# Optimization experiments

Measured on AMD Instinct MI355X. Metric: run time of the kernel, lower is better.

The kernel has to match this reference:

```python
import math
import jax, jax.numpy as jnp
import numpy as np

D, H, NB, L, K = 45, 256, 6, 2, 8          # features, hidden, maf blocks, made hidden layers, spline bins
M = 3 * K - 1                               # params per feature (tails='linear')
TAIL = -math.log(1e-6)                      # tail_bound = -log(alpha)
MIN_BW = MIN_BH = MIN_D = 1e-3


def _masks():
    # nflows MADE sequential degrees (random_mask=False)
    d_in = np.arange(1, D + 1)
    d_h = (np.arange(H) % (D - 1)) + 1
    m0 = (d_h[:, None] >= d_in[None, :]).astype(np.float32)   # [H, D]
    mh = (d_h[:, None] >= d_h[None, :]).astype(np.float32)    # [H, H]
    d_out = np.repeat(d_in, M)                                 # nflows tile(): each degree repeated M times
    mf = (d_out[:, None] > d_h[None, :]).astype(np.float32)   # [D*M, H], strict for output layer
    return jnp.asarray(m0), jnp.asarray(mh), jnp.asarray(mf)


def _rq_spline(x, params):
    # x: [B, D]; params: [B, D, M]. unconstrained_rational_quadratic_spline, tails='linear'.
    uw = params[..., :K] / math.sqrt(H)        # nflows divides by sqrt(hidden_features)
    uh = params[..., K:2 * K] / math.sqrt(H)
    const = math.log(math.exp(1.0 - MIN_D) - 1.0)
    ud = jnp.pad(params[..., 2 * K:], ((0, 0), (0, 0), (1, 1)), constant_values=const)  # [B,D,K+1]
    inside = (x >= -TAIL) & (x <= TAIL)
    xc = jnp.clip(x, -TAIL, TAIL)

    def bin_edges(u, mn):
        p = jax.nn.softmax(u, -1)
        p = mn + (1.0 - mn * K) * p
        c = jnp.pad(jnp.cumsum(p, -1), ((0, 0), (0, 0), (1, 0)))
        c = 2.0 * TAIL * c - TAIL
        c = c.at[..., 0].set(-TAIL).at[..., -1].set(TAIL)
        return c, c[..., 1:] - c[..., :-1]

    cw, w = bin_edges(uw, MIN_BW)              # cumwidths [B,D,K+1], widths [B,D,K]
    ch, h = bin_edges(uh, MIN_BH)
    d = MIN_D + jax.nn.softplus(ud)            # derivatives [B,D,K+1]

    idx = jnp.clip(jnp.sum((xc[..., None] >= cw), -1) - 1, 0, K - 1)[..., None]
    g = lambda a: jnp.take_along_axis(a, idx, -1)[..., 0]
    icw, ibw, ich, ih = g(cw[..., :-1]), g(w), g(ch[..., :-1]), g(h)
    idelta = g(h / w)
    id0, id1 = g(d[..., :-1]), g(d[..., 1:])

    th = (xc - icw) / ibw
    th1 = th * (1.0 - th)
    den = idelta + (id0 + id1 - 2.0 * idelta) * th1
    y = ich + ih * (idelta * th * th + id0 * th1) / den
    lad = jnp.log(idelta * idelta * (id1 * th * th + 2.0 * idelta * th1 + id0 * (1.0 - th) ** 2)) - 2.0 * jnp.log(den)
    return jnp.where(inside, y, x), jnp.where(inside, lad, 0.0)


def setup_inputs() -> dict:
    key = jax.random.key(0)
    ks = jax.random.split(key, 10)
    B, s = 32768, 0.02
    return {
        "x": jax.random.normal(ks[0], (B, D), jnp.float32),
        "cond": jax.random.normal(ks[1], (B, 1), jnp.float32),
        "W0": jax.random.normal(ks[2], (NB, H, D), jnp.float32) * s,
        "b0": jax.random.normal(ks[3], (NB, H), jnp.float32) * s,
        "Wc": jax.random.normal(ks[4], (NB, H, 1), jnp.float32) * s,
        "bc": jax.random.normal(ks[5], (NB, H), jnp.float32) * s,
        "Wh": jax.random.normal(ks[6], (NB, L, H, H), jnp.float32) * s,
        "bh": jax.random.normal(ks[7], (NB, L, H), jnp.float32) * s,
        "Wf": jax.random.normal(ks[8], (NB, D * M, H), jnp.float32) * s,
        "bf": jax.random.normal(ks[9], (NB, D * M), jnp.float32) * s,
    }


def reference(x, cond, W0, b0, Wc, bc, Wh, bh, Wf, bf):
    m0, mh, mf = _masks()
    z = x
    ld = jnp.zeros(x.shape[0], x.dtype)
    for b in range(NB):  # CompositeTransform of NB MAF blocks
        hid = z @ (W0[b] * m0).T + b0[b] + cond @ Wc[b].T + bc[b]
        for l in range(L):  # MaskedFeedforwardBlock: linear -> ReLU (dropout=0, no BN)
            hid = jax.nn.relu(hid @ (Wh[b, l] * mh).T + bh[b, l])
        params = (hid @ (Wf[b] * mf).T + bf[b]).reshape(z.shape[0], D, M)
        z, lad = _rq_spline(z, params)
        ld = ld + lad.sum(-1)
    log_z = 0.5 * D * math.log(2.0 * math.pi)
    return -0.5 * jnp.sum(z * z, axis=1) - log_z + ld
```

## Files before the change

### kernel.cpp

```cpp
#include <hip/hip_runtime.h>


typedef __bf16 bf16;
typedef __bf16 bf16x8 __attribute__((ext_vector_type(8)));
typedef float  f32x16 __attribute__((ext_vector_type(16)));

#define TAILF  13.815510557964274f
#define LOGZ   41.352233994210265f

#define WS_W0M   0
#define WS_WHM   196608
#define WS_WFM   1769472
#define WS_BEFF  5210112
#define WS_BFP   5216256
#define WS_WCC   5243136
#define WS_BHP   5249280
#define WS_NEED  5261568

#define N_W0  (6*256*64)
#define N_WH  (6*2*256*256)
#define N_WF  (6*5*224*256)
#define N_PREP (N_W0 + N_WH + N_WF)

__device__ __forceinline__ int s_deg(int s) {
    return (s < 216) ? (s / 6) : (36 + (s - 216) / 5);
}
__device__ __forceinline__ int s_orig(int s) {
    int d, rk;
    if (s < 216) { d = s / 6; rk = s - d * 6; }
    else { int u = s - 216; d = 36 + u / 5; rk = u - (u / 5) * 5; }
    return d + 44 * rk;
}

__global__ void prep_all(const float* __restrict__ W0, const float* __restrict__ b0,
                         const float* __restrict__ Wc, const float* __restrict__ bc,
                         const float* __restrict__ Wh, const float* __restrict__ Wf,
                         const float* __restrict__ bfv, const float* __restrict__ bh,
                         bf16* __restrict__ W0m, bf16* __restrict__ Whm,
                         bf16* __restrict__ Wfm,
                         float* __restrict__ beff, float* __restrict__ bfp,
                         float* __restrict__ Wcc, float* __restrict__ bhp)
{
    int idx = blockIdx.x * 256 + threadIdx.x;
    if (idx < N_W0) {
        int j = idx & 7, lane = (idx >> 3) & 63, chunk = idx >> 9;
        int kt = chunk & 3, cg = (chunk >> 2) & 7, b = chunk >> 5;
        int col = cg * 32 + (lane & 31);
        int k   = kt * 16 + (lane >> 5) * 8 + j;
        int o   = s_orig(col);
        float v = 0.f;
        if (k < 45 && s_deg(col) >= k)
            v = W0[(b * 256 + o) * 45 + k];
        W0m[idx] = (bf16)v;
        if (k == 0) {
            beff[b * 256 + col] = b0[b * 256 + o] + bc[b * 256 + o];
            Wcc[b * 256 + col]  = Wc[b * 256 + o];
        }
    } else if (idx < N_W0 + N_WH) {
        int id = idx - N_W0;
        int j = id & 7, lane = (id >> 3) & 63, chunk = id >> 9;
        int kt = chunk & 15, cg = (chunk >> 4) & 7, bl = chunk >> 7;
        int col = cg * 32 + (lane & 31);
        int k   = kt * 16 + (lane >> 5) * 8 + j;
        int oc  = s_orig(col), ok = s_orig(k);
        float v = (s_deg(col) >= s_deg(k)) ? Wh[bl * 65536 + oc * 256 + ok] : 0.f;
        Whm[id] = (bf16)v;
        if (k == 0)
            bhp[bl * 256 + col] = bh[bl * 256 + oc];
    } else if (idx < N_PREP) {
        int id = idx - (N_W0 + N_WH);
        int j = id & 7, lane = (id >> 3) & 63, chunk = id >> 9;
        int kt = chunk & 15, t2 = chunk >> 4;
        int cg = t2 % 7, bg = t2 / 7;
        int b  = bg / 5, g = bg - 5 * b;
        int col = cg * 32 + (lane & 31);
        int k   = kt * 16 + (lane >> 5) * 8 + j;
        int ok  = s_orig(k);
        int f   = 9 * g + col / 23;
        int m   = col - (col / 23) * 23;
        bool valid = (col < 207);
        float v = 0.f;
        if (valid && (f > s_deg(k)))
            v = Wf[(b * 1035 + f * 23 + m) * 256 + ok];
        Wfm[id] = (bf16)v;
        if (k == 0)
            bfp[bg * 224 + col] = valid ? bfv[b * 1035 + f * 23 + m] : 0.f;
    }
}

#define SO_ZF    0
#define SO_ZB    11776
#define SO_HIDA  18944
#define SO_PBUF  52736
#define SO_COND  80528
#define SO_LD    80784
#define SMEM_BYTES 81040

#define PBF 1544

#define E2(c0,h0,k0,c1,h1,k1) \
    ( (unsigned)(((k0)<<8)|((h0)<<5)|(c0)) | ((unsigned)(((k1)<<8)|((h1)<<5)|(c1))<<16) )

__constant__ unsigned SCHED_IN[8] = {
    E2(6,0,3, 0,0,1), E2(6,1,3, 0,1,1), E2(7,0,3, 1,0,1), E2(7,1,3, 1,1,1),
    E2(3,0,2, 2,0,1), E2(3,1,2, 2,1,1), E2(4,0,2, 5,0,2), E2(4,1,2, 5,1,2)
};
__constant__ unsigned SCHED_HID[8] = {
    E2(7,0,16, 0,0,3), E2(7,1,16, 0,1,3), E2(6,0,15, 1,0,5), E2(6,1,15, 1,1,5),
    E2(5,0,12, 2,0,6), E2(5,1,12, 2,1,6), E2(4,0,11, 3,0,9), E2(4,1,11, 3,1,9)
};
__constant__ unsigned SCHED_OUT[5][8] = {
  { E2(4,0,3, 0,0,1),  E2(4,1,3, 0,1,1),  E2(5,0,3, 1,0,1),  E2(5,1,3, 1,1,1),
    E2(6,0,3, 31,0,0), E2(6,1,3, 31,0,0), E2(2,0,2, 2,1,2),  E2(3,0,2, 3,1,2) },
  { E2(5,0,7, 0,0,4),  E2(5,1,7, 0,1,4),  E2(6,0,7, 31,0,0), E2(6,1,7, 31,0,0),
    E2(3,0,6, 1,0,5),  E2(3,1,6, 1,1,5),  E2(4,0,6, 2,0,5),  E2(4,1,6, 2,1,5) },
  { E2(5,0,10, 0,0,8), E2(5,1,10, 0,1,8), E2(6,0,10, 1,0,8), E2(6,1,10, 1,1,8),
    E2(2,0,9, 2,1,9),  E2(3,0,9, 3,1,9),  E2(4,0,9, 31,0,0), E2(4,1,9, 31,0,0) },
  { E2(5,0,14, 0,0,11),E2(5,1,14, 0,1,11),E2(6,0,14, 31,0,0),E2(6,1,14, 31,0,0),
    E2(4,0,13, 1,0,11),E2(4,1,13, 1,1,11),E2(2,0,12, 2,1,12),E2(3,0,12, 3,1,12) },
  { E2(3,0,16, 0,0,14),E2(3,1,16, 0,1,14),E2(4,0,16, 1,0,15),E2(4,1,16, 1,1,15),
    E2(5,0,16, 2,0,15),E2(5,1,16, 2,1,15),E2(6,0,16, 31,0,0),E2(6,1,16, 31,0,0) }
};

template<int MODE>
__device__ __forceinline__ void epi32(const f32x16& acc, int cg, int hf,
    const float* __restrict__ bias, const float* __restrict__ wcol,
    const float* condl, bf16* dst, int l31, int kh8)
{
    const int col = cg * 32 + l31;
    if (MODE == 2 && col >= 207) return;
    const float bv = bias[col];
    const int rb = (kh8 >> 1) + hf * 32;
    if (MODE == 2) {
        const int fl = col / 23, m = col - fl * 23;
        bf16* dp = dst + fl * PBF + m;
        #pragma unroll
        for (int r = 0; r < 16; ++r) {
            int row = (r & 3) + 8 * (r >> 2) + rb;
            dp[row * 24] = (bf16)(acc[r] + bv);
        }
    } else {
        const float wcv = (MODE == 0) ? wcol[col] : 0.f;
        #pragma unroll
        for (int r = 0; r < 16; ++r) {
            int row = (r & 3) + 8 * (r >> 2) + rb;
            float v = acc[r] + bv;
            if (MODE == 0) v += condl[row] * wcv;
            if (MODE == 1) v = fmaxf(v, 0.f);
            dst[row * 264 + col] = (bf16)v;
        }
    }
}

template<int KTFULL, int MODE>
__device__ __forceinline__ void gemm32(
    const bf16* Asrc, const int lda,
    const bf16* __restrict__ Wp,
    const float* __restrict__ bias, const float* __restrict__ wcol,
    const float* condl, bf16* dst,
    const unsigned* __restrict__ sched,
    int w, int lane, bool preEpiSync)
{
    const int l31 = lane & 31;
    const int kh8 = (lane >> 5) * 8;
    const unsigned se = sched[__builtin_amdgcn_readfirstlane(w)];
    const int cg0 = se & 31,         hf0 = (se >> 5) & 1,  kt0 = (se >> 8) & 31;
    const int cg1 = (se >> 16) & 31, hf1 = (se >> 21) & 1, kt1 = (se >> 24) & 31;

    f32x16 acc0 = {}, acc1 = {};
    {
        const bf16* Bp = Wp + (size_t)cg0 * (KTFULL * 512) + lane * 8;
        const bf16* Ap = Asrc + (hf0 * 32 + l31) * lda + kh8;
        #pragma unroll 1
        for (int kb = 0; kb < kt0; kb += 4) {
            bf16x8 bq[4], aq[4];
            #pragma unroll
            for (int c = 0; c < 4; ++c) if (kb + c < kt0) {
                bq[c] = *reinterpret_cast<const bf16x8*>(Bp + (kb + c) * 512);
                aq[c] = *reinterpret_cast<const bf16x8*>(Ap + (kb + c) * 16);
            }
            #pragma unroll
            for (int c = 0; c < 4; ++c) if (kb + c < kt0)
                acc0 = __builtin_amdgcn_mfma_f32_32x32x16_bf16(aq[c], bq[c], acc0, 0, 0, 0);
        }
    }
    {
        const bf16* Bp = Wp + (size_t)cg1 * (KTFULL * 512) + lane * 8;
        const bf16* Ap = Asrc + (hf1 * 32 + l31) * lda + kh8;
        #pragma unroll 1
        for (int kb = 0; kb < kt1; kb += 4) {
            bf16x8 bq[4], aq[4];
            #pragma unroll
            for (int c = 0; c < 4; ++c) if (kb + c < kt1) {
                bq[c] = *reinterpret_cast<const bf16x8*>(Bp + (kb + c) * 512);
                aq[c] = *reinterpret_cast<const bf16x8*>(Ap + (kb + c) * 16);
            }
            #pragma unroll
            for (int c = 0; c < 4; ++c) if (kb + c < kt1)
                acc1 = __builtin_amdgcn_mfma_f32_32x32x16_bf16(aq[c], bq[c], acc1, 0, 0, 0);
        }
    }

    if (preEpiSync) __syncthreads();

    if (cg0 != 31) epi32<MODE>(acc0, cg0, hf0, bias, wcol, condl, dst, l31, kh8);
    if (cg1 != 31) epi32<MODE>(acc1, cg1, hf1, bias, wcol, condl, dst, l31, kh8);
    __syncthreads();
}

__device__ __forceinline__ void do_spline9(int fb, float* zf, bf16* zb,
                                           const bf16* pbuf, int t, float& lad_acc)
{
    #pragma unroll 1
    for (int task = t; task < 576; task += 512) {
        int fl = task >> 6, r = task & 63;
        const bf16* pp = pbuf + fl * PBF + r * 24;
        bf16x8 q0 = *reinterpret_cast<const bf16x8*>(pp);
        bf16x8 q1 = *reinterpret_cast<const bf16x8*>(pp + 8);
        bf16x8 q2 = *reinterpret_cast<const bf16x8*>(pp + 16);
        float P[23];
        #pragma unroll
        for (int m = 0; m < 8; ++m) P[m]      = (float)q0[m];
        #pragma unroll
        for (int m = 0; m < 8; ++m) P[8 + m]  = (float)q1[m];
        #pragma unroll
        for (int m = 0; m < 7; ++m) P[16 + m] = (float)q2[m];

        float xin = zf[r * 46 + fb + fl];
        float xc  = fminf(fmaxf(xin, -TAILF), TAILF);
        bool inside = (xin >= -TAILF) && (xin <= TAILF);

        float mw = P[0];
        #pragma unroll
        for (int i = 1; i < 8; ++i) mw = fmaxf(mw, P[i]);
        float ew[8], sw = 0.f;
        #pragma unroll
        for (int i = 0; i < 8; ++i) { ew[i] = __expf((P[i] - mw) * 0.0625f); sw += ew[i]; }
        float rws = 0.992f / sw;
        float cw[9]; cw[0] = -TAILF;
        #pragma unroll
        for (int i = 0; i < 8; ++i)
            cw[i + 1] = cw[i] + 2.f * TAILF * (1e-3f + ew[i] * rws);
        cw[8] = TAILF;
        float wb[8];
        #pragma unroll
        for (int i = 0; i < 8; ++i) wb[i] = cw[i + 1] - cw[i];

        float mh = P[8];
        #pragma unroll
        for (int i = 1; i < 8; ++i) mh = fmaxf(mh, P[8 + i]);
        float eh[8], sh = 0.f;
        #pragma unroll
        for (int i = 0; i < 8; ++i) { eh[i] = __expf((P[8 + i] - mh) * 0.0625f); sh += eh[i]; }
        float rhs = 0.992f / sh;
        float ch[9]; ch[0] = -TAILF;
        #pragma unroll
        for (int i = 0; i < 8; ++i)
            ch[i + 1] = ch[i] + 2.f * TAILF * (1e-3f + eh[i] * rhs);
        ch[8] = TAILF;
        float hb[8];
        #pragma unroll
        for (int i = 0; i < 8; ++i) hb[i] = ch[i + 1] - ch[i];

        float dd[9];
        dd[0] = 1.0f; dd[8] = 1.0f;
        #pragma unroll
        for (int i = 1; i < 8; ++i)
            dd[i] = 1e-3f + __logf(1.f + __expf(P[15 + i]));

        float icw = cw[0], ich = ch[0], ibw = wb[0], ibh = hb[0];
        float id0 = dd[0], id1 = dd[1];
        #pragma unroll
        for (int i = 1; i < 8; ++i) {
            bool ge = xc >= cw[i];
            icw = ge ? cw[i] : icw;  ich = ge ? ch[i] : ich;
            ibw = ge ? wb[i] : ibw;  ibh = ge ? hb[i] : ibh;
            id0 = ge ? dd[i] : id0;  id1 = ge ? dd[i + 1] : id1;
        }

        float th  = (xc - icw) / ibw;
        float th1 = th * (1.f - th);
        float dl  = ibh / ibw;
        float den = dl + (id0 + id1 - 2.f * dl) * th1;
        float yy  = ich + ibh * (dl * th * th + id0 * th1) / den;
        float num = dl * dl * (id1 * th * th + 2.f * dl * th1
                               + id0 * (1.f - th) * (1.f - th));
        float lad = __logf(num) - 2.f * __logf(den);

        if (inside) {
            zf[r * 46 + fb + fl] = yy;
            zb[r * 56 + fb + fl] = (bf16)yy;
        }
        lad_acc += inside ? lad : 0.f;
    }
}

__global__ __launch_bounds__(512, 4) void maf_main(
    const float* __restrict__ x, const float* __restrict__ cond,
    const bf16* __restrict__ W0m, const bf16* __restrict__ Whm,
    const bf16* __restrict__ Wfm,
    const float* __restrict__ beff, const float* __restrict__ bfp,
    const float* __restrict__ Wcc, const float* __restrict__ bhp,
    float* __restrict__ out, int B)
{
    extern __shared__ char smem[];
    float* zf    = (float*)(smem + SO_ZF);
    bf16*  zb    = (bf16*)(smem + SO_ZB);
    bf16*  hidA  = (bf16*)(smem + SO_HIDA);
    bf16*  pbuf  = (bf16*)(smem + SO_PBUF);
    float* condl = (float*)(smem + SO_COND);
    float* ldl   = (float*)(smem + SO_LD);

    const int t    = threadIdx.x;
    const int r0   = blockIdx.x * 64;
    const int w    = t >> 6;
    const int lane = t & 63;

    for (int i = t; i < 64 * 11; i += 512) {
        int r = i / 11, c = i - (i / 11) * 11;
        zb[r * 56 + 45 + c] = (bf16)0.f;
    }
    for (int i = t; i < 64 * 45; i += 512) {
        int r = i / 45, f = i - (i / 45) * 45;
        float v = (r0 + r < B) ? x[(size_t)(r0 + r) * 45 + f] : 0.f;
        zf[r * 46 + f] = v;
        zb[r * 56 + f] = (bf16)v;
    }
    if (t < 64) {
        condl[t] = (r0 + t < B) ? cond[r0 + t] : 0.f;
        ldl[t]   = 0.f;
    }
    __syncthreads();

    float lad_acc = 0.f;

    #pragma unroll 1
    for (int b = 0; b < 6; ++b) {
        gemm32<4, 0>(zb, 56, W0m + b * 16384,
                     beff + b * 256, Wcc + b * 256, condl,
                     hidA, SCHED_IN, w, lane, false);
        #pragma unroll 1
        for (int l = 0; l < 2; ++l)
            gemm32<16, 1>(hidA, 264, Whm + (b * 2 + l) * 65536,
                          bhp + (b * 2 + l) * 256, nullptr, condl,
                          hidA, SCHED_HID, w, lane, true);
        #pragma unroll 1
        for (int g = 0; g < 5; ++g) {
            gemm32<16, 2>(hidA, 264, Wfm + (size_t)(b * 5 + g) * 57344,
                          bfp + (b * 5 + g) * 224, nullptr, condl,
                          pbuf, SCHED_OUT[g], w, lane, false);
            do_spline9(g * 9, zf, zb, pbuf, t, lad_acc);
            __syncthreads();
        }
    }

    atomicAdd(&ldl[t & 63], lad_acc);
    __syncthreads();

    if (t < 64 && r0 + t < B) {
        float s = 0.f;
        #pragma unroll
        for (int f = 0; f < 45; ++f) { float v = zf[t * 46 + f]; s += v * v; }
        out[r0 + t] = -0.5f * s - LOGZ + ldl[t];
    }
}

extern "C" void kernel_launch(void* const* d_in, const int* in_sizes, int n_in,
                              void* d_out, int out_size, void* d_ws, size_t ws_size,
                              hipStream_t stream)
{
    const float* x    = (const float*)d_in[0];
    const float* cond = (const float*)d_in[1];
    const float* W0   = (const float*)d_in[2];
    const float* b0   = (const float*)d_in[3];
    const float* Wc   = (const float*)d_in[4];
    const float* bc   = (const float*)d_in[5];
    const float* Wh   = (const float*)d_in[6];
    const float* bh   = (const float*)d_in[7];
    const float* Wf   = (const float*)d_in[8];
    const float* bfv  = (const float*)d_in[9];
    float* out = (float*)d_out;

    const int B = in_sizes[0] / 45;
    if (ws_size < (size_t)WS_NEED) return;

    char* ws = (char*)d_ws;
    bf16*  W0m  = (bf16*)(ws + WS_W0M);
    bf16*  Whm  = (bf16*)(ws + WS_WHM);
    bf16*  Wfm  = (bf16*)(ws + WS_WFM);
    float* beff = (float*)(ws + WS_BEFF);
    float* bfp  = (float*)(ws + WS_BFP);
    float* Wcc  = (float*)(ws + WS_WCC);
    float* bhp  = (float*)(ws + WS_BHP);

    prep_all<<<(N_PREP + 255) / 256, 256, 0, stream>>>(
        W0, b0, Wc, bc, Wh, Wf, bfv, bh, W0m, Whm, Wfm, beff, bfp, Wcc, bhp);

    (void)hipFuncSetAttribute((const void*)maf_main,
                              hipFuncAttributeMaxDynamicSharedMemorySize,
                              SMEM_BYTES);

    const int nwg = (B + 63) / 64;
    maf_main<<<nwg, 512, SMEM_BYTES, stream>>>(
        x, cond, W0m, Whm, Wfm, beff, bfp, Wcc, bhp, out, B);
}
```

Baseline: 366.9 us.

## Assign each wave a full 64-row column tile and software-pipeline B loads

Replaces the balanced per-wave schedule of two independent 32x32 tiles with one 32-column group per wave covering both 32-row halves, so each B fragment loaded from global memory feeds two MFMAs. The k-loop is replaced by a fully unrolled switch that double-buffers B register quads, issuing the next quad's loads before computing the current one. This halves weight traffic per MFMA and improves latency hiding, but drops the load-balanced schedule tables, so wave work is less even across the masked triangular K extents (waves 6/7 share a column group in the output GEMM).

```diff
diff --git a/kernel.cpp b/kernel.cpp
--- a/kernel.cpp
+++ b/kernel.cpp
@@ -98,29 +98,13 @@
 
 #define PBF 1544
 
-#define E2(c0,h0,k0,c1,h1,k1) \
-    ( (unsigned)(((k0)<<8)|((h0)<<5)|(c0)) | ((unsigned)(((k1)<<8)|((h1)<<5)|(c1))<<16) )
-
-__constant__ unsigned SCHED_IN[8] = {
-    E2(6,0,3, 0,0,1), E2(6,1,3, 0,1,1), E2(7,0,3, 1,0,1), E2(7,1,3, 1,1,1),
-    E2(3,0,2, 2,0,1), E2(3,1,2, 2,1,1), E2(4,0,2, 5,0,2), E2(4,1,2, 5,1,2)
-};
-__constant__ unsigned SCHED_HID[8] = {
-    E2(7,0,16, 0,0,3), E2(7,1,16, 0,1,3), E2(6,0,15, 1,0,5), E2(6,1,15, 1,1,5),
-    E2(5,0,12, 2,0,6), E2(5,1,12, 2,1,6), E2(4,0,11, 3,0,9), E2(4,1,11, 3,1,9)
-};
-__constant__ unsigned SCHED_OUT[5][8] = {
-  { E2(4,0,3, 0,0,1),  E2(4,1,3, 0,1,1),  E2(5,0,3, 1,0,1),  E2(5,1,3, 1,1,1),
-    E2(6,0,3, 31,0,0), E2(6,1,3, 31,0,0), E2(2,0,2, 2,1,2),  E2(3,0,2, 3,1,2) },
-  { E2(5,0,7, 0,0,4),  E2(5,1,7, 0,1,4),  E2(6,0,7, 31,0,0), E2(6,1,7, 31,0,0),
-    E2(3,0,6, 1,0,5),  E2(3,1,6, 1,1,5),  E2(4,0,6, 2,0,5),  E2(4,1,6, 2,1,5) },
-  { E2(5,0,10, 0,0,8), E2(5,1,10, 0,1,8), E2(6,0,10, 1,0,8), E2(6,1,10, 1,1,8),
-    E2(2,0,9, 2,1,9),  E2(3,0,9, 3,1,9),  E2(4,0,9, 31,0,0), E2(4,1,9, 31,0,0) },
-  { E2(5,0,14, 0,0,11),E2(5,1,14, 0,1,11),E2(6,0,14, 31,0,0),E2(6,1,14, 31,0,0),
-    E2(4,0,13, 1,0,11),E2(4,1,13, 1,1,11),E2(2,0,12, 2,1,12),E2(3,0,12, 3,1,12) },
-  { E2(3,0,16, 0,0,14),E2(3,1,16, 0,1,14),E2(4,0,16, 1,0,15),E2(4,1,16, 1,1,15),
-    E2(5,0,16, 2,0,15),E2(5,1,16, 2,1,15),E2(6,0,16, 31,0,0),E2(6,1,16, 31,0,0) }
-};
+__constant__ unsigned char HID_KT[8]    = {4,8,8,12,12,12,16,16};
+__constant__ unsigned char OUT_KT[5][7] = {
+    { 4, 4, 4, 4, 4, 4, 4},
+    { 4, 8, 8, 8, 8, 8, 8},
+    { 8, 8,12,12,12,12,12},
+    {12,12,12,12,16,16,16},
+    {16,16,16,16,16,16,16}};
 
 template<int MODE>
 __device__ __forceinline__ void epi32(const f32x16& acc, int cg, int hf,
@@ -153,58 +137,70 @@
 }
 
 template<int KTFULL, int MODE>
-__device__ __forceinline__ void gemm32(
+__device__ __forceinline__ void gemm64(
     const bf16* Asrc, const int lda,
     const bf16* __restrict__ Wp,
     const float* __restrict__ bias, const float* __restrict__ wcol,
     const float* condl, bf16* dst,
-    const unsigned* __restrict__ sched,
-    int w, int lane, bool preEpiSync)
+    int cg, int kt, int halfmask,
+    int lane, bool preEpiSync)
 {
     const int l31 = lane & 31;
     const int kh8 = (lane >> 5) * 8;
-    const unsigned se = sched[__builtin_amdgcn_readfirstlane(w)];
-    const int cg0 = se & 31,         hf0 = (se >> 5) & 1,  kt0 = (se >> 8) & 31;
-    const int cg1 = (se >> 16) & 31, hf1 = (se >> 21) & 1, kt1 = (se >> 24) & 31;
+    const bf16* Bp  = Wp + (size_t)cg * (KTFULL * 512) + lane * 8;
+    const bf16* Alo = Asrc + l31 * lda + kh8;
+    const bf16* Ahi = Alo + 32 * lda;
 
     f32x16 acc0 = {}, acc1 = {};
-    {
-        const bf16* Bp = Wp + (size_t)cg0 * (KTFULL * 512) + lane * 8;
-        const bf16* Ap = Asrc + (hf0 * 32 + l31) * lda + kh8;
-        #pragma unroll 1
-        for (int kb = 0; kb < kt0; kb += 4) {
-            bf16x8 bq[4], aq[4];
-            #pragma unroll
-            for (int c = 0; c < 4; ++c) if (kb + c < kt0) {
-                bq[c] = *reinterpret_cast<const bf16x8*>(Bp + (kb + c) * 512);
-                aq[c] = *reinterpret_cast<const bf16x8*>(Ap + (kb + c) * 16);
-            }
-            #pragma unroll
-            for (int c = 0; c < 4; ++c) if (kb + c < kt0)
-                acc0 = __builtin_amdgcn_mfma_f32_32x32x16_bf16(aq[c], bq[c], acc0, 0, 0, 0);
-        }
-    }
-    {
-        const bf16* Bp = Wp + (size_t)cg1 * (KTFULL * 512) + lane * 8;
-        const bf16* Ap = Asrc + (hf1 * 32 + l31) * lda + kh8;
-        #pragma unroll 1
-        for (int kb = 0; kb < kt1; kb += 4) {
-            bf16x8 bq[4], aq[4];
-            #pragma unroll
-            for (int c = 0; c < 4; ++c) if (kb + c < kt1) {
-                bq[c] = *reinterpret_cast<const bf16x8*>(Bp + (kb + c) * 512);
-                aq[c] = *reinterpret_cast<const bf16x8*>(Ap + (kb + c) * 16);
-            }
-            #pragma unroll
-            for (int c = 0; c < 4; ++c) if (kb + c < kt1)
-                acc1 = __builtin_amdgcn_mfma_f32_32x32x16_bf16(aq[c], bq[c], acc1, 0, 0, 0);
-        }
-    }
+    bf16x8 pA0, pA1, pA2, pA3, pB0, pB1, pB2, pB3;
+
+#define LB(c)  (*reinterpret_cast<const bf16x8*>(Bp + (c) * 512))
+#define LAL(c) (*reinterpret_cast<const bf16x8*>(Alo + (c) * 16))
+#define LAH(c) (*reinterpret_cast<const bf16x8*>(Ahi + (c) * 16))
+#define CHUNK(breg, c) { \
+    bf16x8 a0_ = LAL(c), a1_ = LAH(c); \
+    acc0 = __builtin_amdgcn_mfma_f32_32x32x16_bf16(a0_, breg, acc0, 0, 0, 0); \
+    acc1 = __builtin_amdgcn_mfma_f32_32x32x16_bf16(a1_, breg, acc1, 0, 0, 0); }
+#define LOADQ(r0, r1, r2, r3, q) { \
+    r0 = LB((q)*4 + 0); r1 = LB((q)*4 + 1); \
+    r2 = LB((q)*4 + 2); r3 = LB((q)*4 + 3); }
+#define COMPQ(r0, r1, r2, r3, q) { \
+    CHUNK(r0, (q)*4 + 0) CHUNK(r1, (q)*4 + 1) \
+    CHUNK(r2, (q)*4 + 2) CHUNK(r3, (q)*4 + 3) }
+
+    const int nq = __builtin_amdgcn_readfirstlane(kt >> 2);
+    switch (nq) {
+    case 1:
+        LOADQ(pA0,pA1,pA2,pA3, 0);
+        COMPQ(pA0,pA1,pA2,pA3, 0);
+        break;
+    case 2:
+        LOADQ(pA0,pA1,pA2,pA3, 0); LOADQ(pB0,pB1,pB2,pB3, 1);
+        COMPQ(pA0,pA1,pA2,pA3, 0); COMPQ(pB0,pB1,pB2,pB3, 1);
+        break;
+    case 3:
+        LOADQ(pA0,pA1,pA2,pA3, 0); LOADQ(pB0,pB1,pB2,pB3, 1);
+        COMPQ(pA0,pA1,pA2,pA3, 0); LOADQ(pA0,pA1,pA2,pA3, 2);
+        COMPQ(pB0,pB1,pB2,pB3, 1); COMPQ(pA0,pA1,pA2,pA3, 2);
+        break;
+    default:
+        LOADQ(pA0,pA1,pA2,pA3, 0); LOADQ(pB0,pB1,pB2,pB3, 1);
+        COMPQ(pA0,pA1,pA2,pA3, 0); LOADQ(pA0,pA1,pA2,pA3, 2);
+        COMPQ(pB0,pB1,pB2,pB3, 1); LOADQ(pB0,pB1,pB2,pB3, 3);
+        COMPQ(pA0,pA1,pA2,pA3, 2); COMPQ(pB0,pB1,pB2,pB3, 3);
+        break;
+    }
+#undef LB
+#undef LAL
+#undef LAH
+#undef CHUNK
+#undef LOADQ
+#undef COMPQ
 
     if (preEpiSync) __syncthreads();
 
-    if (cg0 != 31) epi32<MODE>(acc0, cg0, hf0, bias, wcol, condl, dst, l31, kh8);
-    if (cg1 != 31) epi32<MODE>(acc1, cg1, hf1, bias, wcol, condl, dst, l31, kh8);
+    if (halfmask & 1) epi32<MODE>(acc0, cg, 0, bias, wcol, condl, dst, l31, kh8);
+    if (halfmask & 2) epi32<MODE>(acc1, cg, 1, bias, wcol, condl, dst, l31, kh8);
     __syncthreads();
 }
 
@@ -315,6 +311,7 @@
     const int r0   = blockIdx.x * 64;
     const int w    = t >> 6;
     const int lane = t & 63;
+    const int wu   = __builtin_amdgcn_readfirstlane(w);
 
     for (int i = t; i < 64 * 11; i += 512) {
         int r = i / 11, c = i - (i / 11) * 11;
@@ -334,21 +331,25 @@
 
     float lad_acc = 0.f;
 
+    const int hidKt = HID_KT[wu];
+    const int ocg   = (wu <= 5) ? wu : 6;
+    const int ohm   = (wu <= 5) ? 3 : ((wu == 6) ? 1 : 2);
+
     #pragma unroll 1
     for (int b = 0; b < 6; ++b) {
-        gemm32<4, 0>(zb, 56, W0m + b * 16384,
+        gemm64<4, 0>(zb, 56, W0m + b * 16384,
                      beff + b * 256, Wcc + b * 256, condl,
-                     hidA, SCHED_IN, w, lane, false);
+                     hidA, wu, 4, 3, lane, false);
         #pragma unroll 1
         for (int l = 0; l < 2; ++l)
-            gemm32<16, 1>(hidA, 264, Whm + (b * 2 + l) * 65536,
+            gemm64<16, 1>(hidA, 264, Whm + (b * 2 + l) * 65536,
                           bhp + (b * 2 + l) * 256, nullptr, condl,
-                          hidA, SCHED_HID, w, lane, true);
+                          hidA, wu, hidKt, 3, lane, true);
         #pragma unroll 1
         for (int g = 0; g < 5; ++g) {
-            gemm32<16, 2>(hidA, 264, Wfm + (size_t)(b * 5 + g) * 57344,
+            gemm64<16, 2>(hidA, 264, Wfm + (size_t)(b * 5 + g) * 57344,
                           bfp + (b * 5 + g) * 224, nullptr, condl,
-                          pbuf, SCHED_OUT[g], w, lane, false);
+                          pbuf, ocg, OUT_KT[g][ocg], ohm, lane, false);
             do_spline9(g * 9, zf, zb, pbuf, t, lad_acc);
             __syncthreads();
         }
```

New measurement: 325.6 us. 11.3% less time.
